# Optimization experiments

Measured on AMD Instinct MI355X. Metric: run time of the kernel, lower is better.

Reference implementation:

```python
import jax, jax.numpy as jnp
import numpy as np

N = 8192      # nodes; also input feature dim (x.shape[0] used as in_channels)
E = 524288    # edges per edge type (avg degree 64)
H = 200       # hidden dim (hard-coded in RecomNet)
MEAN_RATING = 3.5


def setup_inputs() -> dict:
    key = jax.random.key(0)
    ks = jax.random.split(key, 14)
    s_in = np.float32(1.0 / np.sqrt(N))
    s_h = np.float32(1.0 / np.sqrt(H))
    return {
        "x": jax.random.normal(ks[0], (N, N), jnp.float32),
        "edge_sim": jax.random.randint(ks[1], (2, E), 0, N),
        "edge_rat": jax.random.randint(ks[2], (2, E), 0, N),
        "mask": jax.random.randint(ks[3], (E,), 0, 2).astype(bool),
        # conv1 params (in=N, out=H)
        "w1_self": jax.random.normal(ks[4], (N, H), jnp.float32) * s_in,
        "w1_sim": jax.random.normal(ks[5], (N, H), jnp.float32) * s_in,
        "w1_rat": jax.random.normal(ks[6], (N, H), jnp.float32) * s_in,
        "b1": jnp.zeros((H,), jnp.float32),
        # conv2 params (in=H, out=H)
        "w2_self": jax.random.normal(ks[7], (H, H), jnp.float32) * s_h,
        "w2_sim": jax.random.normal(ks[8], (H, H), jnp.float32) * s_h,
        "w2_rat": jax.random.normal(ks[9], (H, H), jnp.float32) * s_h,
        "b2": jnp.zeros((H,), jnp.float32),
        # bilinear decoder
        "Q": jax.random.normal(ks[10], (H, H), jnp.float32) * s_h,
    }


def _recom_conv(edge_sim, edge_rat, x, w_self, w_sim, w_rat, b):
    # linear-then-gather-then-scatter (linear commutes with sum aggregation)
    m_sim = (x @ w_sim)[edge_sim[0]]                                   # [E, H]
    agg_sim = jax.ops.segment_sum(m_sim, edge_sim[1], num_segments=N)  # [N, H]
    m_rat = (x @ w_rat)[edge_rat[0]]
    agg_rat = jax.ops.segment_sum(m_rat, edge_rat[1], num_segments=N)
    return x @ w_self + agg_sim + agg_rat + b


def reference(x, w1_self, w1_sim, w1_rat, b1, w2_self, w2_sim, w2_rat, b2, Q,
              edge_sim, edge_rat, mask):
    h = _recom_conv(edge_sim, edge_rat, x, w1_self, w1_sim, w1_rat, b1)
    h = jax.nn.relu(h)
    h = _recom_conv(edge_sim, edge_rat, h, w2_self, w2_sim, w2_rat, b2)
    h1 = h[edge_rat[0]]                                                # [E, H]
    h2 = h[edge_rat[1]]                                                # [E, H]
    pred = jnp.einsum("eh,hk,ek->e", h1, Q, h2) + MEAN_RATING          # [E]
    # original compacts with boolean mask (dynamic shape); here we keep a
    # fixed [E] output and zero out unmasked edges
    return jnp.where(mask, pred, 0.0)
```

## Files before the change

### kernel.cpp

```cpp
#include <hip/hip_runtime.h>

#define NN 8192
#define EE 524288
#define HPAD 256
#define NP 640

using s16x8 = __attribute__((ext_vector_type(8))) short;
using f32x4 = __attribute__((ext_vector_type(4))) float;

__device__ __forceinline__ unsigned short f2b(float f) {
    unsigned u = __float_as_uint(f);
    u = (u + 0x7FFFu + ((u >> 16) & 1u)) >> 16;
    return (unsigned short)u;
}
__device__ __forceinline__ float b2f(unsigned short u) {
    return __uint_as_float((unsigned)u << 16);
}

__device__ __forceinline__ void async16(const unsigned short* g, unsigned short* l)
{
    __builtin_amdgcn_global_load_lds(
        (const __attribute__((address_space(1))) unsigned int*)g,
        (__attribute__((address_space(3))) unsigned int*)l, 16, 0, 0);
}


__global__ void cvt_f2b_kernel(const float* __restrict__ in,
                               unsigned short* __restrict__ out, int n4)
{
    int i = blockIdx.x * 256 + threadIdx.x;
    if (i >= n4) return;
    float4 v = ((const float4*)in)[i];
    ushort4 o;
    o.x = f2b(v.x); o.y = f2b(v.y); o.z = f2b(v.z); o.w = f2b(v.w);
    ((ushort4*)out)[i] = o;
}

__global__ void transpose_w_kernel(const float* __restrict__ w0,
                                   const float* __restrict__ w1,
                                   const float* __restrict__ w2,
                                   unsigned short* __restrict__ out,
                                   int Kout, int Kreal, int Nreal)
{
    __shared__ float tile[32][33];
    const int kb = blockIdx.x << 5;
    const int nb = blockIdx.y << 5;
    const int tx = threadIdx.x, ty = threadIdx.y;
    const int n = nb + tx;
    const float* w = (n < 200) ? w0 : (n < 400) ? w1 : w2;
    const int c = (n < 200) ? n : (n < 400) ? n - 200 : n - 400;
#pragma unroll
    for (int i = 0; i < 4; ++i) {
        const int k = kb + ty + (i << 3);
        float v = 0.f;
        if (n < Nreal && k < Kreal) v = w[(size_t)k * 200 + c];
        tile[ty + (i << 3)][tx] = v;
    }
    __syncthreads();
#pragma unroll
    for (int i = 0; i < 4; ++i) {
        const int nn = nb + ty + (i << 3);
        out[(size_t)nn * Kout + kb + tx] = f2b(tile[tx][ty + (i << 3)]);
    }
}

__global__ __launch_bounds__(256) void gemm_mfma(
    const unsigned short* __restrict__ A,
    const unsigned short* __restrict__ BT,
    float* __restrict__ C, unsigned short* __restrict__ Cb,
    int lda, int KC, int ldc, size_t planeStride)
{
    __shared__ unsigned short As[2][128 * 64];
    __shared__ unsigned short Bs[2][128 * 64];
    const int tid  = threadIdx.x;
    const int lane = tid & 63;
    const int w    = tid >> 6;
    const int row0 = blockIdx.y << 7;
    const int col0 = blockIdx.x << 7;
    const int z    = blockIdx.z;
    const int wm = (w >> 1) << 6;
    const int wn = (w & 1) << 6;

    const int sr = lane >> 3;
    const int sc = (lane & 7) ^ sr;
    const size_t kbase = (size_t)z * KC + ((size_t)sc << 3);
    const unsigned short* aG = A  + (size_t)(row0 + w * 8 + sr) * lda + kbase;
    const unsigned short* bG = BT + (size_t)(col0 + w * 8 + sr) * lda + kbase;
    const int ldsOff = w * 8;

    const f32x4 zero = {0.f, 0.f, 0.f, 0.f};
    f32x4 acc[4][4];
#pragma unroll
    for (int i = 0; i < 4; ++i)
#pragma unroll
        for (int j = 0; j < 4; ++j) acc[i][j] = zero;

#pragma unroll
    for (int it = 0; it < 4; ++it) {
        async16(aG + (size_t)(it * 32) * lda, &As[0][(it * 32 + ldsOff) << 6]);
        async16(bG + (size_t)(it * 32) * lda, &Bs[0][(it * 32 + ldsOff) << 6]);
    }
    __syncthreads();

    const int T = KC >> 6;
    for (int t = 0; t < T; ++t) {
        const int cur = t & 1;
        if (t + 1 < T) {
            const int ko = (t + 1) << 6;
#pragma unroll
            for (int it = 0; it < 4; ++it) {
                async16(aG + (size_t)(it * 32) * lda + ko,
                        &As[cur ^ 1][(it * 32 + ldsOff) << 6]);
                async16(bG + (size_t)(it * 32) * lda + ko,
                        &Bs[cur ^ 1][(it * 32 + ldsOff) << 6]);
            }
        }
#pragma unroll
        for (int kk = 0; kk < 2; ++kk) {
            const int q  = (kk << 2) + (lane >> 4);
            const int sl = (q ^ (lane & 7)) << 3;
            s16x8 af[4], bfv[4];
#pragma unroll
            for (int i = 0; i < 4; ++i) {
                const int rm = wm + (i << 4) + (lane & 15);
                af[i]  = *(const s16x8*)(&As[cur][(rm << 6) + sl]);
                const int rn = wn + (i << 4) + (lane & 15);
                bfv[i] = *(const s16x8*)(&Bs[cur][(rn << 6) + sl]);
            }
#pragma unroll
            for (int i = 0; i < 4; ++i)
#pragma unroll
                for (int j = 0; j < 4; ++j)
                    acc[i][j] = __builtin_amdgcn_mfma_f32_16x16x32_bf16(
                        af[i], bfv[j], acc[i][j], 0, 0, 0);
        }
        __syncthreads();
    }

    const int cr = (lane >> 4) << 2;
    const int cc = lane & 15;
    if (Cb) {
#pragma unroll
        for (int i = 0; i < 4; ++i)
#pragma unroll
            for (int j = 0; j < 4; ++j)
#pragma unroll
                for (int r = 0; r < 4; ++r)
                    Cb[(size_t)(row0 + wm + (i << 4) + cr + r) * ldc
                       + (col0 + wn + (j << 4) + cc)] = f2b(acc[i][j][r]);
    } else {
        float* Cp = C + (size_t)z * planeStride;
#pragma unroll
        for (int i = 0; i < 4; ++i)
#pragma unroll
            for (int j = 0; j < 4; ++j)
#pragma unroll
                for (int r = 0; r < 4; ++r)
                    Cp[(size_t)(row0 + wm + (i << 4) + cr + r) * ldc
                       + (col0 + wn + (j << 4) + cc)] = acc[i][j][r];
    }
}

__global__ void combine_kernel(const float* __restrict__ p0,
                               const float* __restrict__ p1,
                               float* __restrict__ y_self,
                               unsigned short* __restrict__ y_simb,
                               unsigned short* __restrict__ y_ratb)
{
    int t = blockIdx.x * 256 + threadIdx.x;
    int n = t / 50, j4 = (t - n * 50) << 2;
    const float* a = p0 + (size_t)n * NP;
    float4 s = *(const float4*)(a + j4);
    float4 m = *(const float4*)(a + 200 + j4);
    float4 r = *(const float4*)(a + 400 + j4);
    if (p1) {
        const float* b = p1 + (size_t)n * NP;
        float4 s2 = *(const float4*)(b + j4);
        float4 m2 = *(const float4*)(b + 200 + j4);
        float4 r2 = *(const float4*)(b + 400 + j4);
        s.x += s2.x; s.y += s2.y; s.z += s2.z; s.w += s2.w;
        m.x += m2.x; m.y += m2.y; m.z += m2.z; m.w += m2.w;
        r.x += r2.x; r.y += r2.y; r.z += r2.z; r.w += r2.w;
    }
    *(float4*)(y_self + (size_t)n * 200 + j4) = s;
    ushort4 mo, ro;
    mo.x = f2b(m.x); mo.y = f2b(m.y); mo.z = f2b(m.z); mo.w = f2b(m.w);
    ro.x = f2b(r.x); ro.y = f2b(r.y); ro.z = f2b(r.z); ro.w = f2b(r.w);
    *(ushort4*)(y_simb + (size_t)n * 200 + j4) = mo;
    *(ushort4*)(y_ratb + (size_t)n * 200 + j4) = ro;
}


__global__ void hist_kernel(const int* __restrict__ edges, int* __restrict__ deg)
{
    int e = blockIdx.x * 256 + threadIdx.x;
    if (e < EE) atomicAdd(&deg[edges[EE + e]], 1);
}

__global__ void scan_kernel(const int* __restrict__ deg,
                            int* __restrict__ off, int* __restrict__ pos)
{
    __shared__ int part[256];
    const int t = threadIdx.x;
    const int base = t * 32;
    int s = 0;
#pragma unroll
    for (int i = 0; i < 32; ++i) s += deg[base + i];
    part[t] = s;
    __syncthreads();
    for (int d = 1; d < 256; d <<= 1) {
        int v = (t >= d) ? part[t - d] : 0;
        __syncthreads();
        part[t] += v;
        __syncthreads();
    }
    int run = (t == 0) ? 0 : part[t - 1];
    for (int i = 0; i < 32; ++i) {
        off[base + i] = run;
        pos[base + i] = run;
        run += deg[base + i];
    }
    if (t == 255) off[NN] = run;
}

__global__ void reorder_kernel(const int* __restrict__ edges,
                               int* __restrict__ pos, int2* __restrict__ se)
{
    int e = blockIdx.x * 256 + threadIdx.x;
    if (e >= EE) return;
    int p = atomicAdd(&pos[edges[EE + e]], 1);
    se[p] = make_int2(edges[e], e);
}

__global__ __launch_bounds__(256) void agg_pass_kernel(
    const unsigned short* __restrict__ msg,
    const int* __restrict__ off, const int2* __restrict__ se,
    const float* __restrict__ y_self, const float* __restrict__ bias,
    float* __restrict__ h, unsigned short* __restrict__ hb, int relu)
{
    __shared__ float part[4][200];
    const int n = blockIdx.x;
    const int w = threadIdx.x >> 6;
    const int lane = threadIdx.x & 63;
    const int j4 = lane << 2;
    const bool act = lane < 50;

    float4 acc = {0.f, 0.f, 0.f, 0.f};
    const int e1 = off[n + 1];
    for (int i = off[n] + w; i < e1; i += 4) {
        const int src = se[i].x;
        if (act) {
            ushort4 v = *(const ushort4*)(msg + (size_t)src * 200 + j4);
            acc.x += b2f(v.x); acc.y += b2f(v.y);
            acc.z += b2f(v.z); acc.w += b2f(v.w);
        }
    }
    if (act) *(float4*)&part[w][j4] = acc;
    __syncthreads();
    const int j = threadIdx.x;
    if (j < 200) {
        float v = part[0][j] + part[1][j] + part[2][j] + part[3][j];
        if (y_self) v += y_self[(size_t)n * 200 + j] + bias[j];
        else        v += h[(size_t)n * 200 + j];
        if (relu) v = fmaxf(v, 0.f);
        if (hb) hb[((size_t)n << 8) + j] = f2b(v);
        else    h[(size_t)n * 200 + j] = v;
    } else if (hb && j < HPAD) {
        hb[((size_t)n << 8) + j] = 0;
    }
}

__global__ __launch_bounds__(256) void pred_kernel(
    const unsigned short* __restrict__ hQb,
    const unsigned short* __restrict__ h2b,
    const int* __restrict__ off, const int2* __restrict__ se,
    const int* __restrict__ mask, float* __restrict__ out)
{
    const int n = blockIdx.x;
    const int w = threadIdx.x >> 6;
    const int lane = threadIdx.x & 63;
    float4 b = {0.f, 0.f, 0.f, 0.f};
    if (lane < 50) {
        ushort4 v = *(const ushort4*)(h2b + ((size_t)n << 8) + (lane << 2));
        b.x = b2f(v.x); b.y = b2f(v.y); b.z = b2f(v.z); b.w = b2f(v.w);
    }
    const int e1 = off[n + 1];
    for (int i = off[n] + w; i < e1; i += 4) {
        const int2 p = ((const int2*)se)[i];
        float s = 0.f;
        if (lane < 50) {
            ushort4 a = *(const ushort4*)(hQb + ((size_t)p.x << 8) + (lane << 2));
            s = fmaf(b2f(a.x), b.x, fmaf(b2f(a.y), b.y,
                fmaf(b2f(a.z), b.z, b2f(a.w) * b.w)));
        }
#pragma unroll
        for (int o = 32; o > 0; o >>= 1) s += __shfl_down(s, o, 64);
        if (lane == 0) out[p.y] = mask[p.y] ? (s + 3.5f) : 0.f;
    }
}

extern "C" void kernel_launch(void* const* d_in, const int* in_sizes, int n_in,
                              void* d_out, int out_size, void* d_ws, size_t ws_size,
                              hipStream_t stream)
{
    const float* x       = (const float*)d_in[0];
    const int*   e_sim   = (const int*)d_in[1];
    const int*   e_rat   = (const int*)d_in[2];
    const int*   mask    = (const int*)d_in[3];
    const float* w1_self = (const float*)d_in[4];
    const float* w1_sim  = (const float*)d_in[5];
    const float* w1_rat  = (const float*)d_in[6];
    const float* b1      = (const float*)d_in[7];
    const float* w2_self = (const float*)d_in[8];
    const float* w2_sim  = (const float*)d_in[9];
    const float* w2_rat  = (const float*)d_in[10];
    const float* b2      = (const float*)d_in[11];
    const float* Q       = (const float*)d_in[12];
    float* out = (float*)d_out;

    char* p = (char*)d_ws;
    auto alloc = [&](size_t bytes) -> char* {
        char* r = p;
        p += (bytes + 255) & ~(size_t)255;
        return r;
    };
    unsigned short* xb    = (unsigned short*)alloc((size_t)NN * NN * 2);
    unsigned short* wbT1  = (unsigned short*)alloc((size_t)NP * NN * 2);
    unsigned short* wbT2  = (unsigned short*)alloc((size_t)NP * HPAD * 2);
    unsigned short* QT    = (unsigned short*)alloc((size_t)HPAD * HPAD * 2);
    float* ypart = (float*)alloc((size_t)2 * NN * NP * 4);
    float* y_self = (float*)alloc((size_t)NN * 200 * 4);
    unsigned short* y_simb = (unsigned short*)alloc((size_t)NN * 200 * 2);
    unsigned short* y_ratb = (unsigned short*)alloc((size_t)NN * 200 * 2);
    float* h1  = (float*)alloc((size_t)NN * 200 * 4);
    float* h2  = (float*)alloc((size_t)NN * 200 * 4);
    unsigned short* h1b = (unsigned short*)alloc((size_t)NN * HPAD * 2);
    unsigned short* h2b = (unsigned short*)alloc((size_t)NN * HPAD * 2);
    unsigned short* hQb = (unsigned short*)alloc((size_t)NN * HPAD * 2);
    int* deg_sim = (int*)alloc(NN * 4);
    int* deg_rat = (int*)alloc(NN * 4);
    int* off_sim = (int*)alloc((NN + 1) * 4);
    int* off_rat = (int*)alloc((NN + 1) * 4);
    int* pos_sim = (int*)alloc(NN * 4);
    int* pos_rat = (int*)alloc(NN * 4);
    int2* se_sim = (int2*)alloc((size_t)EE * 8);
    int2* se_rat = (int2*)alloc((size_t)EE * 8);

    const dim3 blk(256);
    const dim3 tblk(32, 8);

    cvt_f2b_kernel<<<(NN * NN / 4) / 256, blk, 0, stream>>>(x, xb, NN * NN / 4);
    transpose_w_kernel<<<dim3(NN / 32, NP / 32), tblk, 0, stream>>>(
        w1_self, w1_sim, w1_rat, wbT1, NN, NN, 600);
    transpose_w_kernel<<<dim3(HPAD / 32, NP / 32), tblk, 0, stream>>>(
        w2_self, w2_sim, w2_rat, wbT2, HPAD, 200, 600);
    transpose_w_kernel<<<dim3(HPAD / 32, HPAD / 32), tblk, 0, stream>>>(
        Q, Q, Q, QT, HPAD, 200, 200);

    hipMemsetAsync(deg_sim, 0, 2 * NN * 4, stream);
    hist_kernel<<<EE / 256, blk, 0, stream>>>(e_sim, deg_sim);
    hist_kernel<<<EE / 256, blk, 0, stream>>>(e_rat, deg_rat);
    scan_kernel<<<1, blk, 0, stream>>>(deg_sim, off_sim, pos_sim);
    scan_kernel<<<1, blk, 0, stream>>>(deg_rat, off_rat, pos_rat);
    reorder_kernel<<<EE / 256, blk, 0, stream>>>(e_sim, pos_sim, se_sim);
    reorder_kernel<<<EE / 256, blk, 0, stream>>>(e_rat, pos_rat, se_rat);

    gemm_mfma<<<dim3(NP / 128, NN / 128, 2), blk, 0, stream>>>(
        xb, wbT1, ypart, nullptr, NN, NN / 2, NP, (size_t)NN * NP);
    combine_kernel<<<NN * 50 / 256, blk, 0, stream>>>(
        ypart, ypart + (size_t)NN * NP, y_self, y_simb, y_ratb);
    agg_pass_kernel<<<NN, blk, 0, stream>>>(y_simb, off_sim, se_sim,
                                            y_self, b1, h1, nullptr, 0);
    agg_pass_kernel<<<NN, blk, 0, stream>>>(y_ratb, off_rat, se_rat,
                                            nullptr, nullptr, h1, h1b, 1);

    gemm_mfma<<<dim3(NP / 128, NN / 128, 1), blk, 0, stream>>>(
        h1b, wbT2, ypart, nullptr, HPAD, HPAD, NP, 0);
    combine_kernel<<<NN * 50 / 256, blk, 0, stream>>>(
        ypart, nullptr, y_self, y_simb, y_ratb);
    agg_pass_kernel<<<NN, blk, 0, stream>>>(y_simb, off_sim, se_sim,
                                            y_self, b2, h2, nullptr, 0);
    agg_pass_kernel<<<NN, blk, 0, stream>>>(y_ratb, off_rat, se_rat,
                                            nullptr, nullptr, h2, h2b, 0);

    gemm_mfma<<<dim3(HPAD / 128, NN / 128, 1), blk, 0, stream>>>(
        h2b, QT, nullptr, hQb, HPAD, HPAD, HPAD, 0);
    pred_kernel<<<NN, blk, 0, stream>>>(hQb, h2b, off_rat, se_rat, mask, out);
}
```

Baseline: 976.1 us.

## Fuse sim/rat aggregation passes, batch graph preprocessing, unroll gathers, remap GEMM blocks

Merges the two per-layer aggregation kernels into one that accumulates both edge types and writes bf16 output directly. This removes the fp32 h intermediate round trip and one launch per layer. Histogram, scan and reorder for both edge types now run as single launches using an extra grid dimension. Edge gather loops in aggregation and prediction are unrolled by four to keep more loads in flight, and the GEMM block index is remapped so that consecutive blocks are spread across XCD-strided groups for cache locality.

```diff
diff --git a/kernel.cpp b/kernel.cpp
--- a/kernel.cpp
+++ b/kernel.cpp
@@ -75,8 +75,16 @@
     const int tid  = threadIdx.x;
     const int lane = tid & 63;
     const int w    = tid >> 6;
-    const int row0 = blockIdx.y << 7;
-    const int col0 = blockIdx.x << 7;
+
+    const int nx   = gridDim.x;
+    const int flat = blockIdx.y * nx + blockIdx.x;
+    const int cpx  = (nx * gridDim.y) >> 3;
+    const int orig = (flat & 7) * cpx + (flat >> 3);
+    const int by   = orig / nx;
+    const int bx   = orig - by * nx;
+
+    const int row0 = by << 7;
+    const int col0 = bx << 7;
     const int z    = blockIdx.z;
     const int wm = (w >> 1) << 6;
     const int wn = (w & 1) << 6;
@@ -191,15 +199,23 @@
 }
 
 
-__global__ void hist_kernel(const int* __restrict__ edges, int* __restrict__ deg)
-{
+__global__ void hist_kernel(const int* __restrict__ e0, const int* __restrict__ e1,
+                            int* __restrict__ d0, int* __restrict__ d1)
+{
+    const int* edges = blockIdx.y ? e1 : e0;
+    int* deg = blockIdx.y ? d1 : d0;
     int e = blockIdx.x * 256 + threadIdx.x;
     if (e < EE) atomicAdd(&deg[edges[EE + e]], 1);
 }
 
-__global__ void scan_kernel(const int* __restrict__ deg,
-                            int* __restrict__ off, int* __restrict__ pos)
-{
+__global__ void scan_kernel(const int* __restrict__ deg0, int* __restrict__ off0,
+                            int* __restrict__ pos0,
+                            const int* __restrict__ deg1, int* __restrict__ off1,
+                            int* __restrict__ pos1)
+{
+    const int* deg = blockIdx.x ? deg1 : deg0;
+    int* off = blockIdx.x ? off1 : off0;
+    int* pos = blockIdx.x ? pos1 : pos0;
     __shared__ int part[256];
     const int t = threadIdx.x;
     const int base = t * 32;
@@ -223,20 +239,61 @@
     if (t == 255) off[NN] = run;
 }
 
-__global__ void reorder_kernel(const int* __restrict__ edges,
-                               int* __restrict__ pos, int2* __restrict__ se)
-{
+__global__ void reorder_kernel(const int* __restrict__ e0, int* __restrict__ pos0,
+                               int2* __restrict__ se0,
+                               const int* __restrict__ e1, int* __restrict__ pos1,
+                               int2* __restrict__ se1)
+{
+    const int* edges = blockIdx.y ? e1 : e0;
+    int* pos = blockIdx.y ? pos1 : pos0;
+    int2* se = blockIdx.y ? se1 : se0;
     int e = blockIdx.x * 256 + threadIdx.x;
     if (e >= EE) return;
     int p = atomicAdd(&pos[edges[EE + e]], 1);
     se[p] = make_int2(edges[e], e);
 }
 
-__global__ __launch_bounds__(256) void agg_pass_kernel(
+
+__device__ __forceinline__ void edge_accum(
     const unsigned short* __restrict__ msg,
     const int* __restrict__ off, const int2* __restrict__ se,
+    int n, int w, int j4, bool act, float4& acc)
+{
+    const int e1 = off[n + 1];
+    int i = off[n] + w;
+    for (; i + 12 < e1; i += 16) {
+        const int s0 = se[i].x;
+        const int s1 = se[i + 4].x;
+        const int s2 = se[i + 8].x;
+        const int s3 = se[i + 12].x;
+        if (act) {
+            ushort4 v0 = *(const ushort4*)(msg + (size_t)s0 * 200 + j4);
+            ushort4 v1 = *(const ushort4*)(msg + (size_t)s1 * 200 + j4);
+            ushort4 v2 = *(const ushort4*)(msg + (size_t)s2 * 200 + j4);
+            ushort4 v3 = *(const ushort4*)(msg + (size_t)s3 * 200 + j4);
+            acc.x += (b2f(v0.x) + b2f(v1.x)) + (b2f(v2.x) + b2f(v3.x));
+            acc.y += (b2f(v0.y) + b2f(v1.y)) + (b2f(v2.y) + b2f(v3.y));
+            acc.z += (b2f(v0.z) + b2f(v1.z)) + (b2f(v2.z) + b2f(v3.z));
+            acc.w += (b2f(v0.w) + b2f(v1.w)) + (b2f(v2.w) + b2f(v3.w));
+        }
+    }
+    for (; i < e1; i += 4) {
+        const int s = se[i].x;
+        if (act) {
+            ushort4 v = *(const ushort4*)(msg + (size_t)s * 200 + j4);
+            acc.x += b2f(v.x); acc.y += b2f(v.y);
+            acc.z += b2f(v.z); acc.w += b2f(v.w);
+        }
+    }
+}
+
+__global__ __launch_bounds__(256) void agg_fused_kernel(
+    const unsigned short* __restrict__ msg_sim,
+    const unsigned short* __restrict__ msg_rat,
+    const int* __restrict__ off_sim, const int2* __restrict__ se_sim,
+    const int* __restrict__ off_rat, const int2* __restrict__ se_rat,
     const float* __restrict__ y_self, const float* __restrict__ bias,
-    float* __restrict__ h, unsigned short* __restrict__ hb, int relu)
+    unsigned short* __restrict__ hb, int relu)
 {
     __shared__ float part[4][200];
     const int n = blockIdx.x;
@@ -246,26 +303,18 @@
     const bool act = lane < 50;
 
     float4 acc = {0.f, 0.f, 0.f, 0.f};
-    const int e1 = off[n + 1];
-    for (int i = off[n] + w; i < e1; i += 4) {
-        const int src = se[i].x;
-        if (act) {
-            ushort4 v = *(const ushort4*)(msg + (size_t)src * 200 + j4);
-            acc.x += b2f(v.x); acc.y += b2f(v.y);
-            acc.z += b2f(v.z); acc.w += b2f(v.w);
-        }
-    }
+    edge_accum(msg_sim, off_sim, se_sim, n, w, j4, act, acc);
+    edge_accum(msg_rat, off_rat, se_rat, n, w, j4, act, acc);
+
     if (act) *(float4*)&part[w][j4] = acc;
     __syncthreads();
     const int j = threadIdx.x;
     if (j < 200) {
-        float v = part[0][j] + part[1][j] + part[2][j] + part[3][j];
-        if (y_self) v += y_self[(size_t)n * 200 + j] + bias[j];
-        else        v += h[(size_t)n * 200 + j];
+        float v = part[0][j] + part[1][j] + part[2][j] + part[3][j]
+                + y_self[(size_t)n * 200 + j] + bias[j];
         if (relu) v = fmaxf(v, 0.f);
-        if (hb) hb[((size_t)n << 8) + j] = f2b(v);
-        else    h[(size_t)n * 200 + j] = v;
-    } else if (hb && j < HPAD) {
+        hb[((size_t)n << 8) + j] = f2b(v);
+    } else if (j < HPAD) {
         hb[((size_t)n << 8) + j] = 0;
     }
 }
@@ -285,8 +334,43 @@
         b.x = b2f(v.x); b.y = b2f(v.y); b.z = b2f(v.z); b.w = b2f(v.w);
     }
     const int e1 = off[n + 1];
-    for (int i = off[n] + w; i < e1; i += 4) {
-        const int2 p = ((const int2*)se)[i];
+    int i = off[n] + w;
+    for (; i + 12 < e1; i += 16) {
+        const int2 p0 = se[i];
+        const int2 p1 = se[i + 4];
+        const int2 p2 = se[i + 8];
+        const int2 p3 = se[i + 12];
+        float s0 = 0.f, s1 = 0.f, s2 = 0.f, s3 = 0.f;
+        if (lane < 50) {
+            ushort4 a0 = *(const ushort4*)(hQb + ((size_t)p0.x << 8) + (lane << 2));
+            ushort4 a1 = *(const ushort4*)(hQb + ((size_t)p1.x << 8) + (lane << 2));
+            ushort4 a2 = *(const ushort4*)(hQb + ((size_t)p2.x << 8) + (lane << 2));
+            ushort4 a3 = *(const ushort4*)(hQb + ((size_t)p3.x << 8) + (lane << 2));
+            s0 = fmaf(b2f(a0.x), b.x, fmaf(b2f(a0.y), b.y,
+                 fmaf(b2f(a0.z), b.z, b2f(a0.w) * b.w)));
+            s1 = fmaf(b2f(a1.x), b.x, fmaf(b2f(a1.y), b.y,
+                 fmaf(b2f(a1.z), b.z, b2f(a1.w) * b.w)));
+            s2 = fmaf(b2f(a2.x), b.x, fmaf(b2f(a2.y), b.y,
+                 fmaf(b2f(a2.z), b.z, b2f(a2.w) * b.w)));
+            s3 = fmaf(b2f(a3.x), b.x, fmaf(b2f(a3.y), b.y,
+                 fmaf(b2f(a3.z), b.z, b2f(a3.w) * b.w)));
+        }
+#pragma unroll
+        for (int o = 32; o > 0; o >>= 1) {
+            s0 += __shfl_down(s0, o, 64);
+            s1 += __shfl_down(s1, o, 64);
+            s2 += __shfl_down(s2, o, 64);
+            s3 += __shfl_down(s3, o, 64);
+        }
+        if (lane == 0) {
+            out[p0.y] = mask[p0.y] ? (s0 + 3.5f) : 0.f;
+            out[p1.y] = mask[p1.y] ? (s1 + 3.5f) : 0.f;
+            out[p2.y] = mask[p2.y] ? (s2 + 3.5f) : 0.f;
+            out[p3.y] = mask[p3.y] ? (s3 + 3.5f) : 0.f;
+        }
+    }
+    for (; i < e1; i += 4) {
+        const int2 p = se[i];
         float s = 0.f;
         if (lane < 50) {
             ushort4 a = *(const ushort4*)(hQb + ((size_t)p.x << 8) + (lane << 2));
@@ -332,8 +416,6 @@
     float* y_self = (float*)alloc((size_t)NN * 200 * 4);
     unsigned short* y_simb = (unsigned short*)alloc((size_t)NN * 200 * 2);
     unsigned short* y_ratb = (unsigned short*)alloc((size_t)NN * 200 * 2);
-    float* h1  = (float*)alloc((size_t)NN * 200 * 4);
-    float* h2  = (float*)alloc((size_t)NN * 200 * 4);
     unsigned short* h1b = (unsigned short*)alloc((size_t)NN * HPAD * 2);
     unsigned short* h2b = (unsigned short*)alloc((size_t)NN * HPAD * 2);
     unsigned short* hQb = (unsigned short*)alloc((size_t)NN * HPAD * 2);
@@ -358,30 +440,25 @@
         Q, Q, Q, QT, HPAD, 200, 200);
 
     hipMemsetAsync(deg_sim, 0, 2 * NN * 4, stream);
-    hist_kernel<<<EE / 256, blk, 0, stream>>>(e_sim, deg_sim);
-    hist_kernel<<<EE / 256, blk, 0, stream>>>(e_rat, deg_rat);
-    scan_kernel<<<1, blk, 0, stream>>>(deg_sim, off_sim, pos_sim);
-    scan_kernel<<<1, blk, 0, stream>>>(deg_rat, off_rat, pos_rat);
-    reorder_kernel<<<EE / 256, blk, 0, stream>>>(e_sim, pos_sim, se_sim);
-    reorder_kernel<<<EE / 256, blk, 0, stream>>>(e_rat, pos_rat, se_rat);
+    hist_kernel<<<dim3(EE / 256, 2), blk, 0, stream>>>(e_sim, e_rat, deg_sim, deg_rat);
+    scan_kernel<<<2, blk, 0, stream>>>(deg_sim, off_sim, pos_sim,
+                                       deg_rat, off_rat, pos_rat);
+    reorder_kernel<<<dim3(EE / 256, 2), blk, 0, stream>>>(
+        e_sim, pos_sim, se_sim, e_rat, pos_rat, se_rat);
 
     gemm_mfma<<<dim3(NP / 128, NN / 128, 2), blk, 0, stream>>>(
         xb, wbT1, ypart, nullptr, NN, NN / 2, NP, (size_t)NN * NP);
     combine_kernel<<<NN * 50 / 256, blk, 0, stream>>>(
         ypart, ypart + (size_t)NN * NP, y_self, y_simb, y_ratb);
-    agg_pass_kernel<<<NN, blk, 0, stream>>>(y_simb, off_sim, se_sim,
-                                            y_self, b1, h1, nullptr, 0);
-    agg_pass_kernel<<<NN, blk, 0, stream>>>(y_ratb, off_rat, se_rat,
-                                            nullptr, nullptr, h1, h1b, 1);
+    agg_fused_kernel<<<NN, blk, 0, stream>>>(
+        y_simb, y_ratb, off_sim, se_sim, off_rat, se_rat, y_self, b1, h1b, 1);
 
     gemm_mfma<<<dim3(NP / 128, NN / 128, 1), blk, 0, stream>>>(
         h1b, wbT2, ypart, nullptr, HPAD, HPAD, NP, 0);
     combine_kernel<<<NN * 50 / 256, blk, 0, stream>>>(
         ypart, nullptr, y_self, y_simb, y_ratb);
-    agg_pass_kernel<<<NN, blk, 0, stream>>>(y_simb, off_sim, se_sim,
-                                            y_self, b2, h2, nullptr, 0);
-    agg_pass_kernel<<<NN, blk, 0, stream>>>(y_ratb, off_rat, se_rat,
-                                            nullptr, nullptr, h2, h2b, 0);
+    agg_fused_kernel<<<NN, blk, 0, stream>>>(
+        y_simb, y_ratb, off_sim, se_sim, off_rat, se_rat, y_self, b2, h2b, 0);
 
     gemm_mfma<<<dim3(HPAD / 128, NN / 128, 1), blk, 0, stream>>>(
         h2b, QT, nullptr, hQb, HPAD, HPAD, HPAD, 0);
```

Result: faster. 850.0 us (-12.9%).
